# Kernel tuning notes

Measured on AMD Instinct MI355X. Metric: run time of the kernel, lower is better.

## Reference

```python
import jax, jax.numpy as jnp
import numpy as np

B, CIN, CINT, H, W = 2, 2048, 512, 96, 96
CQK = CINT // 8  # 64, mmcv CrissCrossAttention query/key channels
NG = 32          # GroupNorm groups
EPS = 1e-5


def conv1x1(x, w, b):
    # x: [B,C,H,W], w: [O,C,1,1], b: [O]
    y = jnp.einsum('bchw,oc->bohw', x, w[:, :, 0, 0])
    return y + b[None, :, None, None]


def conv3x3(x, w):
    return jax.lax.conv_general_dilated(
        x, w, window_strides=(1, 1), padding=((1, 1), (1, 1)),
        dimension_numbers=('NCHW', 'OIHW', 'NCHW'))


def group_norm(x, gamma, beta):
    b, c, h, w = x.shape
    xg = x.reshape(b, NG, c // NG, h, w)
    mu = xg.mean(axis=(2, 3, 4), keepdims=True)
    var = xg.var(axis=(2, 3, 4), keepdims=True)
    xg = (xg - mu) * jax.lax.rsqrt(var + EPS)
    return xg.reshape(b, c, h, w) * gamma[None, :, None, None] + beta[None, :, None, None]


def criss_cross_attention(x, qw, qb, kw, kb, vw, vb, gamma):
    # mmcv CrissCrossAttention: attention restricted to each pixel's row + column.
    b, c, h, w = x.shape
    q = conv1x1(x, qw, qb)  # [B,Cqk,H,W]
    k = conv1x1(x, kw, kb)  # [B,Cqk,H,W]
    v = conv1x1(x, vw, vb)  # [B,C,H,W]
    # column (H-direction) energy: e_H[b,h,w,i] = sum_c q[b,c,h,w] k[b,c,i,w]
    e_h = jnp.einsum('bchw,bciw->bhwi', q, k)
    diag = jnp.eye(h, dtype=bool)[:, None, :]  # mask i==h (self counted once, in W branch)
    e_h = jnp.where(diag, -jnp.inf, e_h)
    # row (W-direction) energy: e_W[b,h,w,j] = sum_c q[b,c,h,w] k[b,c,h,j]
    e_w = jnp.einsum('bchw,bchj->bhwj', q, k)
    attn = jax.nn.softmax(jnp.concatenate([e_h, e_w], axis=-1), axis=-1)  # [B,H,W,H+W]
    a_h, a_w = attn[..., :h], attn[..., h:]
    out = jnp.einsum('bciw,bhwi->bchw', v, a_h) + jnp.einsum('bchj,bhwj->bchw', v, a_w)
    return gamma * out + x


def setup_inputs() -> dict:
    key = jax.random.key(0)
    ks = jax.random.split(key, 12)
    s = 0.02
    return {
        'x': jax.random.normal(ks[0], (B, CIN, H, W), jnp.float32),
        'conv1_w': jax.random.normal(ks[1], (CINT, CIN, 1, 1), jnp.float32) * s,
        'conv1_b': jnp.zeros((CINT,), jnp.float32),
        'q_w': jax.random.normal(ks[2], (CQK, CINT, 1, 1), jnp.float32) * s,
        'q_b': jnp.zeros((CQK,), jnp.float32),
        'k_w': jax.random.normal(ks[3], (CQK, CINT, 1, 1), jnp.float32) * s,
        'k_b': jnp.zeros((CQK,), jnp.float32),
        'v_w': jax.random.normal(ks[4], (CINT, CINT, 1, 1), jnp.float32) * s,
        'v_b': jnp.zeros((CINT,), jnp.float32),
        'gamma': jnp.asarray(0.5, jnp.float32),
        'convout_w': jax.random.normal(ks[5], (CINT, CINT, 3, 3), jnp.float32) * s,
        'gn_gamma': jnp.ones((CINT,), jnp.float32),
        'gn_beta': jnp.zeros((CINT,), jnp.float32),
    }


def reference(x, conv1_w, conv1_b, q_w, q_b, k_w, k_b, v_w, v_b, gamma,
              convout_w, gn_gamma, gn_beta):
    out = conv1x1(x, conv1_w, conv1_b)
    for _ in range(2):  # recurrence = 2
        out = criss_cross_attention(out, q_w, q_b, k_w, k_b, v_w, v_b, gamma)
    out = conv3x3(out, convout_w)  # ConvModule with GN => conv has no bias
    out = group_norm(out, gn_gamma, gn_beta)
    return out
```

## Files before the change

kernel.cpp:

```cpp
#include <hip/hip_runtime.h>
#include <hip/hip_bf16.h>


typedef __bf16 bf8_t __attribute__((ext_vector_type(8)));
typedef float f32x4 __attribute__((ext_vector_type(4)));

union I4B8 { int4 i; bf8_t b; };

typedef const __attribute__((address_space(1))) void as1_cvoid;
typedef __attribute__((address_space(3))) void as3_void;
__device__ __forceinline__ void gload16(const void* g, void* l) {
  __builtin_amdgcn_global_load_lds((as1_cvoid*)g, (as3_void*)l, 16, 0, 0);
}
__device__ __forceinline__ int rot8(int c, int key) { return (c + key) & 7; }

__global__ __launch_bounds__(256) void cast_rot_k(const float* s, __bf16* d, int K8, int total8) {
  int idx = blockIdx.x * 256 + threadIdx.x;
  if (idx >= total8) return;
  int c8 = idx % K8, n = idx / K8;
  int pos = rot8(c8 & 7, n & 7);
  const float* sp = s + ((long long)n * K8 + c8) * 8;
  float4 a = *(const float4*)sp, b = *(const float4*)(sp + 4);
  I4B8 u;
  u.b[0] = (__bf16)a.x; u.b[1] = (__bf16)a.y; u.b[2] = (__bf16)a.z; u.b[3] = (__bf16)a.w;
  u.b[4] = (__bf16)b.x; u.b[5] = (__bf16)b.y; u.b[6] = (__bf16)b.z; u.b[7] = (__bf16)b.w;
  *(int4*)(d + ((long long)n * K8 + (c8 & ~7) + pos) * 8) = u.i;
}

__global__ __launch_bounds__(256) void wqkv_rot_k(const float* qw, const float* kw, const float* vw, __bf16* d) {
  int idx = blockIdx.x * 256 + threadIdx.x;
  if (idx >= 640 * 64) return;
  int c8 = idx & 63, n = idx >> 6;
  const float* src = (n < 64) ? qw + (long long)n * 512
                   : (n < 128) ? kw + (long long)(n - 64) * 512
                               : vw + (long long)(n - 128) * 512;
  int pos = rot8(c8 & 7, n & 7);
  const float* sp = src + c8 * 8;
  float4 a = *(const float4*)sp, b = *(const float4*)(sp + 4);
  I4B8 u;
  u.b[0] = (__bf16)a.x; u.b[1] = (__bf16)a.y; u.b[2] = (__bf16)a.z; u.b[3] = (__bf16)a.w;
  u.b[4] = (__bf16)b.x; u.b[5] = (__bf16)b.y; u.b[6] = (__bf16)b.z; u.b[7] = (__bf16)b.w;
  *(int4*)(d + ((long long)n * 64 + (c8 & ~7) + pos) * 8) = u.i;
}

__global__ __launch_bounds__(256) void fuse_bias_k(const float* qb, const float* kb, const float* vb,
                                                   float* d, float* stats) {
  int i = blockIdx.x * 256 + threadIdx.x;
  if (i < 128) stats[i] = 0.f;
  if (i >= 640) return;
  d[i] = (i < 64) ? qb[i] : (i < 128) ? kb[i - 64] : vb[i - 128];
}

__global__ __launch_bounds__(256) void reorder_w_k(const float* w, __bf16* wr) {
  __shared__ float ls[4608];
  int o = blockIdx.x;
  int t = threadIdx.x;
  const float* base = w + (long long)o * 4608;
#pragma unroll
  for (int i = 0; i < 18; i++) ls[t + i * 256] = base[t + i * 256];
  __syncthreads();
#pragma unroll
  for (int i = 0; i < 3; i++) {
    int q = t + i * 256;
    if (q >= 576) break;
    int k0 = q * 8;
    int dydx = k0 / 512, c0 = k0 & 511;
    I4B8 u;
#pragma unroll
    for (int j = 0; j < 8; j++) u.b[j] = (__bf16)ls[(c0 + j) * 9 + dydx];
    int pos = rot8((k0 >> 3) & 7, o & 7);
    *(int4*)(wr + (long long)o * 4608 + (k0 & ~63) + pos * 8) = u.i;
  }
}

__global__ __launch_bounds__(256) void transpose_x_k(const float* x, __bf16* xt) {
  __shared__ __bf16 l[64 * 66];
  int c0 = blockIdx.x * 64, s0 = blockIdx.y * 64, b = blockIdx.z;
  int t = threadIdx.x;
#pragma unroll
  for (int i = 0; i < 2; i++) {
    int slot = t + i * 256;
    int cl = slot >> 3, sch = slot & 7;
    const float* src = x + ((long long)(b * 2048 + c0 + cl)) * 9216 + s0 + sch * 8;
    float4 a = *(const float4*)src, bb = *(const float4*)(src + 4);
    __bf16* dst = &l[cl * 66 + sch * 8];
    dst[0] = (__bf16)a.x; dst[1] = (__bf16)a.y; dst[2] = (__bf16)a.z; dst[3] = (__bf16)a.w;
    dst[4] = (__bf16)bb.x; dst[5] = (__bf16)bb.y; dst[6] = (__bf16)bb.z; dst[7] = (__bf16)bb.w;
  }
  __syncthreads();
#pragma unroll
  for (int i = 0; i < 2; i++) {
    int slot = t + i * 256;
    int sl = slot >> 3, cch = slot & 7;
    I4B8 u;
#pragma unroll
    for (int j = 0; j < 8; j++) u.b[j] = l[(cch * 8 + j) * 66 + sl];
    *(int4*)(xt + ((long long)(b * 9216 + s0 + sl)) * 2048 + c0 + rot8(cch, sl & 7) * 8) = u.i;
  }
}

__global__ __launch_bounds__(256) void border0_k(__bf16* padb) {
  int idx = blockIdx.x * 256 + threadIdx.x;
  if (idx >= 776 * 64) return;
  int ch = idx & 63, bi = idx >> 6;
  int b = bi / 388, r = bi % 388;
  int hh, ww;
  if (r < 98) { hh = 0; ww = r; }
  else if (r < 196) { hh = 97; ww = r - 98; }
  else if (r < 292) { hh = r - 196 + 1; ww = 0; }
  else { hh = r - 292 + 1; ww = 97; }
  *(int4*)(padb + ((long long)(b * 9604 + hh * 98 + ww)) * 512 + ch * 8) = make_int4(0, 0, 0, 0);
}

struct GemmAP {
  const __bf16 *A, *B;
  __bf16* C;
  const float* bias;
  long long sAr, sBr, sCr;
  int K, ntn;
};

template <int CROT>
__global__ __launch_bounds__(256) void gemm_async_k(GemmAP p) {
  __shared__ __attribute__((aligned(16))) __bf16 lA[128 * 64];
  __shared__ __attribute__((aligned(16))) __bf16 lB[64 * 64];
  const int t = threadIdx.x;
  const int id = blockIdx.x;
  const int per8 = gridDim.x >> 3;
  const int lin = (id & 7) * per8 + (id >> 3);
  const int m0 = (lin / p.ntn) * 128, n0 = (lin % p.ntn) * 64;
  const int lane = t & 63, wave = t >> 6;
  const int wm = (wave >> 1) * 64, wn = (wave & 1) * 32;
  const int l15 = lane & 15, l4 = lane >> 4;
  const int srow = (lane >> 3), schunk = (lane & 7) * 8;
  f32x4 acc[4][2];
#pragma unroll
  for (int i = 0; i < 4; i++)
#pragma unroll
    for (int j = 0; j < 2; j++) acc[i][j] = f32x4{0.f, 0.f, 0.f, 0.f};

  for (int kb = 0; kb < p.K; kb += 64) {
    const int rbA = wave * 32, rbB = wave * 16;
#pragma unroll
    for (int i = 0; i < 4; i++) {
      int row = rbA + i * 8;
      gload16(p.A + (long long)(m0 + row + srow) * p.sAr + kb + schunk, &lA[row * 64]);
    }
#pragma unroll
    for (int i = 0; i < 2; i++) {
      int row = rbB + i * 8;
      gload16(p.B + (long long)(n0 + row + srow) * p.sBr + kb + schunk, &lB[row * 64]);
    }
    __syncthreads();
#pragma unroll
    for (int kk = 0; kk < 2; kk++) {
      bf8_t af[4], bfr[2];
      int cch = kk * 4 + l4;
#pragma unroll
      for (int mt = 0; mt < 4; mt++) {
        int r = wm + mt * 16 + l15;
        af[mt] = *(bf8_t*)&lA[r * 64 + (rot8(cch, r & 7) << 3)];
      }
#pragma unroll
      for (int nt = 0; nt < 2; nt++) {
        int r = wn + nt * 16 + l15;
        bfr[nt] = *(bf8_t*)&lB[r * 64 + (rot8(cch, r & 7) << 3)];
      }
#pragma unroll
      for (int mt = 0; mt < 4; mt++)
#pragma unroll
        for (int nt = 0; nt < 2; nt++)
          acc[mt][nt] = __builtin_amdgcn_mfma_f32_16x16x32_bf16(af[mt], bfr[nt], acc[mt][nt], 0, 0, 0);
    }
    __syncthreads();
  }
#pragma unroll
  for (int nt = 0; nt < 2; nt++) {
    int col = n0 + wn + nt * 16 + l15;
    float bv = p.bias[col];
#pragma unroll
    for (int mt = 0; mt < 4; mt++) {
      int row0 = m0 + wm + mt * 16 + (l4 << 2);
#pragma unroll
      for (int r = 0; r < 4; r++) {
        int row = row0 + r;
        int pc = CROT ? (col & ~63) + (rot8((col >> 3) & 7, row & 7) << 3) + (col & 7) : col;
        p.C[(long long)row * p.sCr + pc] = (__bf16)(acc[mt][nt][r] + bv);
      }
    }
  }
}

struct AggP {
  const __bf16 *A, *B;
  __bf16* C;
  const __bf16 *tmp, *res;
  const float* gma;
  long long bB1, bB2, sBr;
  long long cB1, cB2, sCr;
};

template <int MODE>
__global__ __launch_bounds__(256) void agg_k(AggP p) {
  __shared__ __attribute__((aligned(16))) __bf16 lA[128 * 64];
  __shared__ __attribute__((aligned(16))) __bf16 lB[128 * 64];
  const int t = threadIdx.x;
  const int z = blockIdx.z;
  const int z1 = z / 96, z2 = z % 96;
  const __bf16* A = p.A + (long long)z * (96 * 128);
  const __bf16* B = p.B + (long long)z1 * p.bB1 + (long long)z2 * p.bB2;
  const int n0 = blockIdx.x * 128;
  const int lane = t & 63, wave = t >> 6;
  const int wm = (wave >> 1) * 64, wn = (wave & 1) * 64;
  const int l15 = lane & 15, l4 = lane >> 4;
  const int srow = lane >> 3, schunk = (lane & 7) * 8;
  f32x4 acc[4][4];
#pragma unroll
  for (int i = 0; i < 4; i++)
#pragma unroll
    for (int j = 0; j < 4; j++) acc[i][j] = f32x4{0.f, 0.f, 0.f, 0.f};

#pragma unroll
  for (int kb = 0; kb < 128; kb += 64) {
    const int rb = wave * 32;
#pragma unroll
    for (int i = 0; i < 4; i++) {
      int row = rb + i * 8;
      gload16(A + (long long)(row + srow) * 128 + kb + schunk, &lA[row * 64]);
    }
#pragma unroll
    for (int i = 0; i < 4; i++) {
      int slot = t + i * 256;
      int kl = slot & 63, cch = slot >> 6;
      int gk = kb + kl;
      I4B8 u;
      u.i = make_int4(0, 0, 0, 0);
      if (gk < 96) u.i = *(const int4*)(B + (long long)gk * p.sBr + n0 + cch * 8);
#pragma unroll
      for (int j = 0; j < 8; j++) {
        int n = cch * 8 + j;
        lB[n * 64 + (rot8(kl >> 3, n & 7) << 3) + (kl & 7)] = u.b[j];
      }
    }
    __syncthreads();
#pragma unroll
    for (int kk = 0; kk < 2; kk++) {
      bf8_t af[4], bfr[4];
      int cch = kk * 4 + l4;
#pragma unroll
      for (int mt = 0; mt < 4; mt++) {
        int r = wm + mt * 16 + l15;
        af[mt] = *(bf8_t*)&lA[r * 64 + (rot8(cch, r & 7) << 3)];
      }
#pragma unroll
      for (int nt = 0; nt < 4; nt++) {
        int r = wn + nt * 16 + l15;
        bfr[nt] = *(bf8_t*)&lB[r * 64 + (rot8(cch, r & 7) << 3)];
      }
#pragma unroll
      for (int mt = 0; mt < 4; mt++)
#pragma unroll
        for (int nt = 0; nt < 4; nt++)
          acc[mt][nt] = __builtin_amdgcn_mfma_f32_16x16x32_bf16(af[mt], bfr[nt], acc[mt][nt], 0, 0, 0);
    }
    __syncthreads();
  }
  long long cbase = (long long)z1 * p.cB1 + (long long)z2 * p.cB2;
  float g = MODE ? *p.gma : 0.f;
#pragma unroll
  for (int nt = 0; nt < 4; nt++) {
    int col = n0 + wn + nt * 16 + l15;
#pragma unroll
    for (int mt = 0; mt < 4; mt++) {
      int row0 = wm + mt * 16 + (l4 << 2);
#pragma unroll
      for (int r = 0; r < 4; r++) {
        int row = row0 + r;
        if (row >= 96) continue;
        long long offL = cbase + (long long)row * p.sCr + col;
        float v = acc[mt][nt][r];
        if (MODE == 0) {
          p.C[offL] = (__bf16)v;
        } else {
          int rc = (col & ~63) + (rot8((col >> 3) & 7, row & 7) << 3) + (col & 7);
          long long offP = cbase + (long long)row * p.sCr + rc;
          v = g * ((float)p.tmp[offL] + v) + (float)p.res[offP];
          if (MODE == 1) {
            p.C[offP] = (__bf16)v;
          } else {
            int pc = (col & ~63) + (rot8((col >> 3) & 7, (row + 1) & 7) << 3) + (col & 7);
            long long pidx = (long long)z1 * 9604 + (long long)(z2 + 1) * 98 + (row + 1);
            p.C[pidx * 512 + pc] = (__bf16)v;
          }
        }
      }
    }
  }
}

__global__ __launch_bounds__(384) void cc_scores_k(const __bf16* qkv, float* attnfH, float* attnfW) {
  __shared__ __attribute__((aligned(16))) __bf16 Qs[96 * 64];
  __shared__ __attribute__((aligned(16))) __bf16 Ks[96 * 64];
  int bfi = blockIdx.x;
  int b = bfi / 96, f = bfi % 96;
  int mode = blockIdx.y;
  long long base = (mode == 0) ? ((long long)(b * 9216 + f)) * 640 : ((long long)(b * 9216 + f * 96)) * 640;
  long long rstr = (mode == 0) ? 96 * 640 : 640;
  int t = threadIdx.x;
#pragma unroll
  for (int i = 0; i < 2; i++) {
    int slot = t + i * 384;
    int r = slot >> 3, c = slot & 7;
    int sw = rot8(c, r & 7) << 3;
    *(int4*)&Qs[r * 64 + sw] = *(const int4*)(qkv + base + (long long)r * rstr + c * 8);
    *(int4*)&Ks[r * 64 + sw] = *(const int4*)(qkv + base + (long long)r * rstr + 64 + c * 8);
  }
  __syncthreads();
  int lane = t & 63, wave = t >> 6;
  int l15 = lane & 15, l4 = lane >> 4;
  f32x4 acc[6];
#pragma unroll
  for (int i = 0; i < 6; i++) acc[i] = f32x4{0.f, 0.f, 0.f, 0.f};
#pragma unroll
  for (int kk = 0; kk < 2; kk++) {
    int ar = wave * 16 + l15;
    int cch = kk * 4 + l4;
    bf8_t af = *(bf8_t*)&Qs[ar * 64 + (rot8(cch, ar & 7) << 3)];
#pragma unroll
    for (int nt = 0; nt < 6; nt++) {
      int br = nt * 16 + l15;
      bf8_t bfr = *(bf8_t*)&Ks[br * 64 + (rot8(cch, br & 7) << 3)];
      acc[nt] = __builtin_amdgcn_mfma_f32_16x16x32_bf16(af, bfr, acc[nt], 0, 0, 0);
    }
  }
  float* dst = (mode == 0 ? attnfH : attnfW) + (long long)bfi * 9216;
#pragma unroll
  for (int nt = 0; nt < 6; nt++) {
#pragma unroll
    for (int r = 0; r < 4; r++) {
      int m = wave * 16 + (l4 << 2) + r;
      int n = nt * 16 + l15;
      float v = acc[nt][r];
      if (mode == 0 && n == m) v = -__builtin_inff();
      dst[m * 96 + n] = v;
    }
  }
}

__global__ __launch_bounds__(256) void cc_softmax_k(const float* attnfH, const float* attnfW,
                                                    __bf16* a_h, __bf16* a_w) {
  int wave = threadIdx.x >> 6, lane = threadIdx.x & 63;
  int pix = blockIdx.x * 4 + wave;
  int b = pix / 9216, hw = pix % 9216;
  int h = hw / 96, w2 = hw % 96;
  const float* ehb = attnfH + ((long long)(b * 96 + w2)) * 9216 + h * 96;
  const float* ewb = attnfW + ((long long)(b * 96 + h)) * 9216 + w2 * 96;
  float x0 = ehb[lane];
  float x1 = lane < 32 ? ehb[64 + lane] : -__builtin_inff();
  float x2 = ewb[lane];
  float x3 = lane < 32 ? ewb[64 + lane] : -__builtin_inff();
  float m = fmaxf(fmaxf(x0, x1), fmaxf(x2, x3));
#pragma unroll
  for (int o = 32; o; o >>= 1) m = fmaxf(m, __shfl_xor(m, o));
  float e0 = __expf(x0 - m), e1 = __expf(x1 - m), e2 = __expf(x2 - m), e3 = __expf(x3 - m);
  float s = e0 + e1 + e2 + e3;
#pragma unroll
  for (int o = 32; o; o >>= 1) s += __shfl_xor(s, o);
  float inv = 1.f / s;
  __bf16* dh = a_h + ((long long)((b * 96 + w2) * 96 + h)) * 128;
  __bf16* dw = a_w + ((long long)((b * 96 + h) * 96 + w2)) * 128;
  int kh = h & 7, kw2 = w2 & 7;
  int k1 = lane, k2 = 64 + lane;
  int p1h = (k1 & ~63) + (rot8((k1 >> 3) & 7, kh) << 3) + (k1 & 7);
  int p2h = (k2 & ~63) + (rot8((k2 >> 3) & 7, kh) << 3) + (k2 & 7);
  int p1w = (k1 & ~63) + (rot8((k1 >> 3) & 7, kw2) << 3) + (k1 & 7);
  int p2w = (k2 & ~63) + (rot8((k2 >> 3) & 7, kw2) << 3) + (k2 & 7);
  dh[p1h] = (__bf16)(e0 * inv);
  dh[p2h] = (__bf16)(lane < 32 ? e1 * inv : 0.f);
  dw[p1w] = (__bf16)(e2 * inv);
  dw[p2w] = (__bf16)(lane < 32 ? e3 * inv : 0.f);
}

__global__ __launch_bounds__(256) void conv3_gemm_k(const __bf16* pin, const __bf16* wr, __bf16* C) {
  __shared__ __attribute__((aligned(16))) __bf16 lA[128 * 64];
  __shared__ __attribute__((aligned(16))) __bf16 lB[128 * 64];
  const int t = threadIdx.x;
  const int id = blockIdx.x;
  const int per8 = gridDim.x >> 3;
  const int lin = (id & 7) * per8 + (id >> 3);
  const int m0 = (lin >> 2) * 128, n0 = (lin & 3) * 128;
  const int lane = t & 63, wave = t >> 6;
  const int wm = (wave >> 1) * 64, wn = (wave & 1) * 64;
  const int l15 = lane & 15, l4 = lane >> 4;
  const int srow = lane >> 3, schunk = (lane & 7) * 8;
  const int rb = wave * 32;
  f32x4 acc[4][4];
#pragma unroll
  for (int i = 0; i < 4; i++)
#pragma unroll
    for (int j = 0; j < 4; j++) acc[i][j] = f32x4{0.f, 0.f, 0.f, 0.f};
  long long sbase[4], bbase[4];
#pragma unroll
  for (int i = 0; i < 4; i++) {
    int r = rb + i * 8 + srow;
    int m = m0 + r;
    int b = m / 9216, hw = m % 9216;
    int h = hw / 96, w2 = hw % 96;
    sbase[i] = ((long long)b * 9604 + h * 98 + w2) * 512 + schunk;
    bbase[i] = (long long)(n0 + r) * 4608 + schunk;
  }
  int w2f[4];
#pragma unroll
  for (int mt = 0; mt < 4; mt++) w2f[mt] = (m0 + wm + mt * 16 + l15) % 96;

  int kt = 0;
  for (int tap = 0; tap < 9; tap++) {
    const int dy = tap / 3, dx = tap - dy * 3;
    const long long aoff = (long long)(dy * 98 + dx) * 512;
    int keyA[4];
#pragma unroll
    for (int mt = 0; mt < 4; mt++) keyA[mt] = (w2f[mt] + dx) & 7;
    for (int sl = 0; sl < 8; sl++, kt++) {
      const int c0k = sl * 64;
#pragma unroll
      for (int i = 0; i < 4; i++) {
        gload16(pin + sbase[i] + aoff + c0k, &lA[(rb + i * 8) * 64]);
        gload16(wr + bbase[i] + kt * 64, &lB[(rb + i * 8) * 64]);
      }
      __syncthreads();
#pragma unroll
      for (int kk = 0; kk < 2; kk++) {
        bf8_t af[4], bfr[4];
        int cch = kk * 4 + l4;
#pragma unroll
        for (int mt = 0; mt < 4; mt++) {
          int r = wm + mt * 16 + l15;
          af[mt] = *(bf8_t*)&lA[r * 64 + (rot8(cch, keyA[mt]) << 3)];
        }
#pragma unroll
        for (int nt = 0; nt < 4; nt++) {
          int r = wn + nt * 16 + l15;
          bfr[nt] = *(bf8_t*)&lB[r * 64 + (rot8(cch, r & 7) << 3)];
        }
#pragma unroll
        for (int mt = 0; mt < 4; mt++)
#pragma unroll
          for (int nt = 0; nt < 4; nt++)
            acc[mt][nt] = __builtin_amdgcn_mfma_f32_16x16x32_bf16(af[mt], bfr[nt], acc[mt][nt], 0, 0, 0);
      }
      __syncthreads();
    }
  }
#pragma unroll
  for (int nt = 0; nt < 4; nt++) {
    int col = n0 + wn + nt * 16 + l15;
#pragma unroll
    for (int mt = 0; mt < 4; mt++) {
      int row0 = m0 + wm + mt * 16 + (l4 << 2);
#pragma unroll
      for (int r = 0; r < 4; r++) {
        int row = row0 + r;
        C[(long long)row * 512 + col] = (__bf16)acc[mt][nt][r];
      }
    }
  }
}

__global__ __launch_bounds__(256) void gn_stats_k(const __bf16* z, float* stats) {
  int bi = blockIdx.x, t = threadIdx.x;
  const __bf16* base = z + (long long)bi * (72 * 512);
  int g = (t & 63) >> 1;
  float s = 0.f, ss = 0.f;
#pragma unroll
  for (int i = 0; i < 18; i++) {
    I4B8 u;
    u.i = *(const int4*)(base + ((long long)(t + i * 256)) * 8);
#pragma unroll
    for (int j = 0; j < 8; j++) {
      float f = (float)u.b[j];
      s += f;
      ss += f * f;
    }
  }
  s += __shfl_xor(s, 1);
  ss += __shfl_xor(ss, 1);
  __shared__ float red[2][4][32];
  int wave = t >> 6, lane = t & 63;
  if (!(lane & 1)) {
    red[0][wave][g] = s;
    red[1][wave][g] = ss;
  }
  __syncthreads();
  if (t < 32) {
    float S = red[0][0][t] + red[0][1][t] + red[0][2][t] + red[0][3][t];
    float SS = red[1][0][t] + red[1][1][t] + red[1][2][t] + red[1][3][t];
    int b = bi >> 7;
    atomicAdd(&stats[2 * (b * 32 + t)], S);
    atomicAdd(&stats[2 * (b * 32 + t) + 1], SS);
  }
}

__global__ __launch_bounds__(256) void gn_write_k(const __bf16* z, const float* stats,
                                                 const float* gng, const float* gnb, float* out) {
  __shared__ __bf16 l[64 * 98];
  int c0 = blockIdx.x * 64, h = blockIdx.y, b = blockIdx.z;
  int t = threadIdx.x;
#pragma unroll
  for (int i = 0; i < 3; i++) {
    int slot = t + i * 256;
    int wl = slot >> 3, cch = slot & 7;
    I4B8 u;
    u.i = *(const int4*)(z + ((long long)(b * 9216 + h * 96 + wl)) * 512 + c0 + cch * 8);
#pragma unroll
    for (int j = 0; j < 8; j++) l[(cch * 8 + j) * 98 + wl] = u.b[j];
  }
  __syncthreads();
  const float inv = 1.f / 147456.f;
#pragma unroll
  for (int i = 0; i < 3; i++) {
    int slot = t + i * 256;
    int wch = slot % 12, cl = slot / 12;
    int c = c0 + cl;
    int g = c >> 4;
    float S = stats[2 * (b * 32 + g)], SS = stats[2 * (b * 32 + g) + 1];
    float mean = S * inv;
    float rstd = rsqrtf(SS * inv - mean * mean + 1e-5f);
    float sc = rstd * gng[c];
    float sh = gnb[c] - mean * sc;
    float4 o0, o1;
    const __bf16* src = &l[cl * 98 + wch * 8];
    o0.x = (float)src[0] * sc + sh; o0.y = (float)src[1] * sc + sh;
    o0.z = (float)src[2] * sc + sh; o0.w = (float)src[3] * sc + sh;
    o1.x = (float)src[4] * sc + sh; o1.y = (float)src[5] * sc + sh;
    o1.z = (float)src[6] * sc + sh; o1.w = (float)src[7] * sc + sh;
    float* dst = out + ((long long)((b * 512 + c) * 96 + h)) * 96 + wch * 8;
    *(float4*)dst = o0;
    *(float4*)(dst + 4) = o1;
  }
}

extern "C" void kernel_launch(void* const* d_in, const int* in_sizes, int n_in,
                              void* d_out, int out_size, void* d_ws, size_t ws_size,
                              hipStream_t stream) {
  (void)in_sizes; (void)n_in; (void)out_size;
  const float* x = (const float*)d_in[0];
  const float* conv1w = (const float*)d_in[1];
  const float* conv1b = (const float*)d_in[2];
  const float* qw = (const float*)d_in[3];
  const float* qbias = (const float*)d_in[4];
  const float* kw = (const float*)d_in[5];
  const float* kbias = (const float*)d_in[6];
  const float* vw = (const float*)d_in[7];
  const float* vbias = (const float*)d_in[8];
  const float* gma = (const float*)d_in[9];
  const float* cow = (const float*)d_in[10];
  const float* gng = (const float*)d_in[11];
  const float* gnb = (const float*)d_in[12];
  float* out = (float*)d_out;

  if (ws_size < 134876160ULL) return;

  char* w = (char*)d_ws;
  __bf16* xt     = (__bf16*)(w);
  __bf16* qkv    = (__bf16*)(w);
  float* attnfH  = (float*)(w + 23592960);
  float* attnfW  = (float*)(w + 30670848);
  __bf16* a_h    = (__bf16*)(w + 37748736);
  __bf16* a_w    = (__bf16*)(w + 42467328);
  __bf16* padb   = (__bf16*)(w + 47185920);
  __bf16* wrot   = (__bf16*)(w + 66854912);
  __bf16* ya     = (__bf16*)(w + 75497472);
  __bf16* yb     = (__bf16*)(w + 94371840);
  __bf16* tmp1   = (__bf16*)(w + 113246208);
  __bf16* zb     = (__bf16*)(w);
  __bf16* c1wb   = (__bf16*)(w + 132120576);
  __bf16* wqkvb  = (__bf16*)(w + 134217728);
  float* qkvbias = (float*)(w + 134873088);
  float* stats   = (float*)(w + 134875648);

  cast_rot_k<<<512, 256, 0, stream>>>(conv1w, c1wb, 256, 131072);
  wqkv_rot_k<<<160, 256, 0, stream>>>(qw, kw, vw, wqkvb);
  fuse_bias_k<<<3, 256, 0, stream>>>(qbias, kbias, vbias, qkvbias, stats);
  transpose_x_k<<<dim3(32, 144, 2), 256, 0, stream>>>(x, xt);

  {
    GemmAP p{};
    p.A = xt; p.B = c1wb; p.C = ya; p.bias = conv1b;
    p.sAr = 2048; p.sBr = 2048; p.sCr = 512;
    p.K = 2048; p.ntn = 8;
    gemm_async_k<1><<<1152, 256, 0, stream>>>(p);
  }

  for (int it = 0; it < 2; it++) {
    __bf16* tin = it ? yb : ya;
    {
      GemmAP p{};
      p.A = tin; p.B = wqkvb; p.C = qkv; p.bias = qkvbias;
      p.sAr = 512; p.sBr = 512; p.sCr = 640;
      p.K = 512; p.ntn = 10;
      gemm_async_k<0><<<1440, 256, 0, stream>>>(p);
    }
    cc_scores_k<<<dim3(192, 2), 384, 0, stream>>>(qkv, attnfH, attnfW);
    cc_softmax_k<<<4608, 256, 0, stream>>>(attnfH, attnfW, a_h, a_w);
    {
      AggP p{};
      p.A = a_h; p.B = qkv + 128; p.C = tmp1;
      p.bB1 = (long long)9216 * 640; p.bB2 = 640; p.sBr = (long long)96 * 640;
      p.cB1 = (long long)9216 * 512; p.cB2 = 512; p.sCr = (long long)96 * 512;
      agg_k<0><<<dim3(4, 1, 192), 256, 0, stream>>>(p);
    }
    {
      AggP p{};
      p.A = a_w; p.B = qkv + 128;
      p.bB1 = (long long)9216 * 640; p.bB2 = (long long)96 * 640; p.sBr = 640;
      p.cB1 = (long long)9216 * 512; p.cB2 = (long long)96 * 512; p.sCr = 512;
      p.tmp = tmp1; p.res = tin; p.gma = gma;
      if (it == 0) {
        p.C = yb;
        agg_k<1><<<dim3(4, 1, 192), 256, 0, stream>>>(p);
      } else {
        p.C = padb;
        agg_k<2><<<dim3(4, 1, 192), 256, 0, stream>>>(p);
      }
    }
  }

  reorder_w_k<<<512, 256, 0, stream>>>(cow, wrot);
  border0_k<<<194, 256, 0, stream>>>(padb);
  conv3_gemm_k<<<576, 256, 0, stream>>>(padb, wrot, zb);
  gn_stats_k<<<256, 256, 0, stream>>>(zb, stats);
  gn_write_k<<<dim3(8, 96, 2), 256, 0, stream>>>(zb, stats, gng, gnb, out);
}
```

Measured before the change: 619.1 us.

## Pre-transpose Q/K/V per column so column attention uses contiguous async loads

Adds a transpose kernel that writes per-column contiguous Q/K rows and a K-major, rotation-swizzled copy of V, padded to 128 along H. The column-direction score kernel now reads Q/K contiguously instead of with a 96×640-element stride. The column aggregation GEMM loads its B tile with async global-to-LDS copies instead of per-element scattered LDS writes. The cost is an extra kernel and extra memory traffic. The new buffers alias workspace regions (a_h, padb), and the V copy's size may extend past padb into the next region.

Result: slower. 633.2 us (+2.3%).

```diff
diff --git a/kernel.cpp b/kernel.cpp
--- a/kernel.cpp
+++ b/kernel.cpp
@@ -110,6 +110,49 @@
   else if (r < 292) { hh = r - 196 + 1; ww = 0; }
   else { hh = r - 292 + 1; ww = 97; }
   *(int4*)(padb + ((long long)(b * 9604 + hh * 98 + ww)) * 512 + ch * 8) = make_int4(0, 0, 0, 0);
+}
+
+__global__ __launch_bounds__(256) void vtrans_k(const __bf16* qkv, __bf16* qkvT, __bf16* vt1) {
+  int bw = blockIdx.x;
+  int b = bw / 96, w2 = bw % 96;
+  int t = threadIdx.x;
+  const __bf16* src = qkv + ((long long)(b * 9216) + w2) * 640;
+  int mode = blockIdx.y;
+  if (mode == 0) {
+#pragma unroll
+    for (int i = 0; i < 6; i++) {
+      int slot = t + i * 256;
+      int h = slot >> 4, c8 = slot & 15;
+      int4 u = *(const int4*)(src + (long long)h * (96 * 640) + c8 * 8);
+      *(int4*)(qkvT + ((long long)bw * 96 + h) * 128 + c8 * 8) = u;
+    }
+    return;
+  }
+  int half = mode - 1;
+  __shared__ __bf16 l[96 * 256];
+#pragma unroll
+  for (int i = 0; i < 12; i++) {
+    int slot = t + i * 256;
+    int h = slot >> 5, c8 = slot & 31;
+    int4 u = *(const int4*)(src + (long long)h * (96 * 640) + 128 + half * 256 + c8 * 8);
+    *(int4*)&l[h * 256 + ((c8 ^ ((h >> 3) & 7)) << 3)] = u;
+  }
+  __syncthreads();
+  __bf16* dst = vt1 + (long long)bw * (512 * 128) + (long long)half * (256 * 128);
+#pragma unroll
+  for (int i = 0; i < 16; i++) {
+    int slot = t + i * 256;
+    int cl = slot >> 4, kc = slot & 15;
+    int c = half * 256 + cl;
+    I4B8 u;
+#pragma unroll
+    for (int j = 0; j < 8; j++) {
+      int h = kc * 8 + j;
+      u.b[j] = (h < 96) ? l[h * 256 + ((((cl >> 3) ^ (kc & 7)) << 3) | (cl & 7))] : (__bf16)0.f;
+    }
+    int pos = (kc & ~7) + rot8(kc & 7, c & 7);
+    *(int4*)(dst + (long long)cl * 128 + pos * 8) = u.i;
+  }
 }
 
 struct GemmAP {
@@ -228,18 +271,27 @@
       int row = rb + i * 8;
       gload16(A + (long long)(row + srow) * 128 + kb + schunk, &lA[row * 64]);
     }
-#pragma unroll
-    for (int i = 0; i < 4; i++) {
-      int slot = t + i * 256;
-      int kl = slot & 63, cch = slot >> 6;
-      int gk = kb + kl;
-      I4B8 u;
-      u.i = make_int4(0, 0, 0, 0);
-      if (gk < 96) u.i = *(const int4*)(B + (long long)gk * p.sBr + n0 + cch * 8);
-#pragma unroll
-      for (int j = 0; j < 8; j++) {
-        int n = cch * 8 + j;
-        lB[n * 64 + (rot8(kl >> 3, n & 7) << 3) + (kl & 7)] = u.b[j];
+    if (MODE == 0) {
+      const __bf16* Bn = B + (long long)n0 * 128;
+#pragma unroll
+      for (int i = 0; i < 4; i++) {
+        int row = rb + i * 8;
+        gload16(Bn + (long long)(row + srow) * 128 + kb + schunk, &lB[row * 64]);
+      }
+    } else {
+#pragma unroll
+      for (int i = 0; i < 4; i++) {
+        int slot = t + i * 256;
+        int kl = slot & 63, cch = slot >> 6;
+        int gk = kb + kl;
+        I4B8 u;
+        u.i = make_int4(0, 0, 0, 0);
+        if (gk < 96) u.i = *(const int4*)(B + (long long)gk * p.sBr + n0 + cch * 8);
+#pragma unroll
+        for (int j = 0; j < 8; j++) {
+          int n = cch * 8 + j;
+          lB[n * 64 + (rot8(kl >> 3, n & 7) << 3) + (kl & 7)] = u.b[j];
+        }
       }
     }
     __syncthreads();
@@ -298,22 +350,25 @@
   }
 }
 
-__global__ __launch_bounds__(384) void cc_scores_k(const __bf16* qkv, float* attnfH, float* attnfW) {
+__global__ __launch_bounds__(384) void cc_scores_k(const __bf16* qkv, const __bf16* qkvT,
+                                                   float* attnfH, float* attnfW) {
   __shared__ __attribute__((aligned(16))) __bf16 Qs[96 * 64];
   __shared__ __attribute__((aligned(16))) __bf16 Ks[96 * 64];
   int bfi = blockIdx.x;
   int b = bfi / 96, f = bfi % 96;
   int mode = blockIdx.y;
-  long long base = (mode == 0) ? ((long long)(b * 9216 + f)) * 640 : ((long long)(b * 9216 + f * 96)) * 640;
-  long long rstr = (mode == 0) ? 96 * 640 : 640;
+  const __bf16* srcb;
+  long long rstr;
+  if (mode == 0) { srcb = qkvT + (long long)bfi * (96 * 128); rstr = 128; }
+  else { srcb = qkv + ((long long)(b * 9216 + f * 96)) * 640; rstr = 640; }
   int t = threadIdx.x;
 #pragma unroll
   for (int i = 0; i < 2; i++) {
     int slot = t + i * 384;
     int r = slot >> 3, c = slot & 7;
     int sw = rot8(c, r & 7) << 3;
-    *(int4*)&Qs[r * 64 + sw] = *(const int4*)(qkv + base + (long long)r * rstr + c * 8);
-    *(int4*)&Ks[r * 64 + sw] = *(const int4*)(qkv + base + (long long)r * rstr + 64 + c * 8);
+    *(int4*)&Qs[r * 64 + sw] = *(const int4*)(srcb + (long long)r * rstr + c * 8);
+    *(int4*)&Ks[r * 64 + sw] = *(const int4*)(srcb + (long long)r * rstr + 64 + c * 8);
   }
   __syncthreads();
   int lane = t & 63, wave = t >> 6;
@@ -566,8 +621,10 @@
   float* attnfH  = (float*)(w + 23592960);
   float* attnfW  = (float*)(w + 30670848);
   __bf16* a_h    = (__bf16*)(w + 37748736);
+  __bf16* qkvT   = (__bf16*)(w + 37748736);
   __bf16* a_w    = (__bf16*)(w + 42467328);
   __bf16* padb   = (__bf16*)(w + 47185920);
+  __bf16* vt1    = (__bf16*)(w + 47185920);
   __bf16* wrot   = (__bf16*)(w + 66854912);
   __bf16* ya     = (__bf16*)(w + 75497472);
   __bf16* yb     = (__bf16*)(w + 94371840);
@@ -600,12 +657,13 @@
       p.K = 512; p.ntn = 10;
       gemm_async_k<0><<<1440, 256, 0, stream>>>(p);
     }
-    cc_scores_k<<<dim3(192, 2), 384, 0, stream>>>(qkv, attnfH, attnfW);
+    vtrans_k<<<dim3(192, 3), 256, 0, stream>>>(qkv, qkvT, vt1);
+    cc_scores_k<<<dim3(192, 2), 384, 0, stream>>>(qkv, qkvT, attnfH, attnfW);
     cc_softmax_k<<<4608, 256, 0, stream>>>(attnfH, attnfW, a_h, a_w);
     {
       AggP p{};
-      p.A = a_h; p.B = qkv + 128; p.C = tmp1;
-      p.bB1 = (long long)9216 * 640; p.bB2 = 640; p.sBr = (long long)96 * 640;
+      p.A = a_h; p.B = vt1; p.C = tmp1;
+      p.bB1 = (long long)96 * 512 * 128; p.bB2 = (long long)512 * 128; p.sBr = 128;
       p.cB1 = (long long)9216 * 512; p.cB2 = 512; p.sCr = (long long)96 * 512;
       agg_k<0><<<dim3(4, 1, 192), 256, 0, stream>>>(p);
     }
```

## Double-buffer LDS tiles in GEMM and conv3x3 kernels with async prefetch

Applied to the files above, without the earlier changes.

Both the generic 1x1 GEMM kernel and the implicit-GEMM 3x3 conv kernel now keep two LDS buffers. Each iteration issues the global-to-LDS loads for the next K slice, then waits only for the current slice with a partial vmcnt. This lets memory latency overlap with MFMA work and drops one full barrier per step. The cost is doubled LDS use (up to 64KB for conv3), which may lower occupancy. Correctness also depends on the hand-written vmcnt counts matching the number of loads issued per stage.

Measured after the change: 693.2 us. +12.0%, slower.

```diff
diff --git a/kernel.cpp b/kernel.cpp
--- a/kernel.cpp
+++ b/kernel.cpp
@@ -122,8 +122,8 @@
 
 template <int CROT>
 __global__ __launch_bounds__(256) void gemm_async_k(GemmAP p) {
-  __shared__ __attribute__((aligned(16))) __bf16 lA[128 * 64];
-  __shared__ __attribute__((aligned(16))) __bf16 lB[64 * 64];
+  __shared__ __attribute__((aligned(16))) __bf16 lA[2][128 * 64];
+  __shared__ __attribute__((aligned(16))) __bf16 lB[2][64 * 64];
   const int t = threadIdx.x;
   const int id = blockIdx.x;
   const int per8 = gridDim.x >> 3;
@@ -133,25 +133,36 @@
   const int wm = (wave >> 1) * 64, wn = (wave & 1) * 32;
   const int l15 = lane & 15, l4 = lane >> 4;
   const int srow = (lane >> 3), schunk = (lane & 7) * 8;
+  const int rbA = wave * 32, rbB = wave * 16;
   f32x4 acc[4][2];
 #pragma unroll
   for (int i = 0; i < 4; i++)
 #pragma unroll
     for (int j = 0; j < 2; j++) acc[i][j] = f32x4{0.f, 0.f, 0.f, 0.f};
 
-  for (int kb = 0; kb < p.K; kb += 64) {
-    const int rbA = wave * 32, rbB = wave * 16;
+  auto stage = [&](int bu, int kb) {
 #pragma unroll
     for (int i = 0; i < 4; i++) {
       int row = rbA + i * 8;
-      gload16(p.A + (long long)(m0 + row + srow) * p.sAr + kb + schunk, &lA[row * 64]);
+      gload16(p.A + (long long)(m0 + row + srow) * p.sAr + kb + schunk, &lA[bu][row * 64]);
     }
 #pragma unroll
     for (int i = 0; i < 2; i++) {
       int row = rbB + i * 8;
-      gload16(p.B + (long long)(n0 + row + srow) * p.sBr + kb + schunk, &lB[row * 64]);
-    }
-    __syncthreads();
+      gload16(p.B + (long long)(n0 + row + srow) * p.sBr + kb + schunk, &lB[bu][row * 64]);
+    }
+  };
+
+  stage(0, 0);
+  int bu = 0;
+  for (int kb = 0; kb < p.K; kb += 64) {
+    if (kb + 64 < p.K) {
+      stage(bu ^ 1, kb + 64);
+      asm volatile("s_waitcnt vmcnt(6)" ::: "memory");
+    } else {
+      asm volatile("s_waitcnt vmcnt(0)" ::: "memory");
+    }
+    __builtin_amdgcn_s_barrier();
 #pragma unroll
     for (int kk = 0; kk < 2; kk++) {
       bf8_t af[4], bfr[2];
@@ -159,12 +170,12 @@
 #pragma unroll
       for (int mt = 0; mt < 4; mt++) {
         int r = wm + mt * 16 + l15;
-        af[mt] = *(bf8_t*)&lA[r * 64 + (rot8(cch, r & 7) << 3)];
+        af[mt] = *(bf8_t*)&lA[bu][r * 64 + (rot8(cch, r & 7) << 3)];
       }
 #pragma unroll
       for (int nt = 0; nt < 2; nt++) {
         int r = wn + nt * 16 + l15;
-        bfr[nt] = *(bf8_t*)&lB[r * 64 + (rot8(cch, r & 7) << 3)];
+        bfr[nt] = *(bf8_t*)&lB[bu][r * 64 + (rot8(cch, r & 7) << 3)];
       }
 #pragma unroll
       for (int mt = 0; mt < 4; mt++)
@@ -172,7 +183,8 @@
         for (int nt = 0; nt < 2; nt++)
           acc[mt][nt] = __builtin_amdgcn_mfma_f32_16x16x32_bf16(af[mt], bfr[nt], acc[mt][nt], 0, 0, 0);
     }
-    __syncthreads();
+    if (kb + 64 < p.K) __builtin_amdgcn_s_barrier();
+    bu ^= 1;
   }
 #pragma unroll
   for (int nt = 0; nt < 2; nt++) {
@@ -382,8 +394,8 @@
 }
 
 __global__ __launch_bounds__(256) void conv3_gemm_k(const __bf16* pin, const __bf16* wr, __bf16* C) {
-  __shared__ __attribute__((aligned(16))) __bf16 lA[128 * 64];
-  __shared__ __attribute__((aligned(16))) __bf16 lB[128 * 64];
+  __shared__ __attribute__((aligned(16))) __bf16 lA[2][128 * 64];
+  __shared__ __attribute__((aligned(16))) __bf16 lB[2][128 * 64];
   const int t = threadIdx.x;
   const int id = blockIdx.x;
   const int per8 = gridDim.x >> 3;
@@ -413,43 +425,55 @@
 #pragma unroll
   for (int mt = 0; mt < 4; mt++) w2f[mt] = (m0 + wm + mt * 16 + l15) % 96;
 
-  int kt = 0;
-  for (int tap = 0; tap < 9; tap++) {
-    const int dy = tap / 3, dx = tap - dy * 3;
-    const long long aoff = (long long)(dy * 98 + dx) * 512;
+  auto stage = [&](int bu, int kt2) {
+    int tap = kt2 >> 3, sl = kt2 & 7;
+    int dyq = tap / 3;
+    long long aoff = (long long)(dyq * 98 + (tap - dyq * 3)) * 512;
+    int c0k = sl * 64;
+#pragma unroll
+    for (int i = 0; i < 4; i++) {
+      gload16(pin + sbase[i] + aoff + c0k, &lA[bu][(rb + i * 8) * 64]);
+      gload16(wr + bbase[i] + kt2 * 64, &lB[bu][(rb + i * 8) * 64]);
+    }
+  };
+
+  stage(0, 0);
+  int bu = 0;
+  for (int kt = 0; kt < 72; kt++) {
+    if (kt < 71) {
+      stage(bu ^ 1, kt + 1);
+      asm volatile("s_waitcnt vmcnt(8)" ::: "memory");
+    } else {
+      asm volatile("s_waitcnt vmcnt(0)" ::: "memory");
+    }
+    __builtin_amdgcn_s_barrier();
+    int tap = kt >> 3;
+    int dx = tap - (tap / 3) * 3;
     int keyA[4];
 #pragma unroll
     for (int mt = 0; mt < 4; mt++) keyA[mt] = (w2f[mt] + dx) & 7;
-    for (int sl = 0; sl < 8; sl++, kt++) {
-      const int c0k = sl * 64;
-#pragma unroll
-      for (int i = 0; i < 4; i++) {
-        gload16(pin + sbase[i] + aoff + c0k, &lA[(rb + i * 8) * 64]);
-        gload16(wr + bbase[i] + kt * 64, &lB[(rb + i * 8) * 64]);
-      }
-      __syncthreads();
-#pragma unroll
-      for (int kk = 0; kk < 2; kk++) {
-        bf8_t af[4], bfr[4];
-        int cch = kk * 4 + l4;
-#pragma unroll
-        for (int mt = 0; mt < 4; mt++) {
-          int r = wm + mt * 16 + l15;
-          af[mt] = *(bf8_t*)&lA[r * 64 + (rot8(cch, keyA[mt]) << 3)];
-        }
-#pragma unroll
-        for (int nt = 0; nt < 4; nt++) {
-          int r = wn + nt * 16 + l15;
-          bfr[nt] = *(bf8_t*)&lB[r * 64 + (rot8(cch, r & 7) << 3)];
-        }
-#pragma unroll
-        for (int mt = 0; mt < 4; mt++)
-#pragma unroll
-          for (int nt = 0; nt < 4; nt++)
-            acc[mt][nt] = __builtin_amdgcn_mfma_f32_16x16x32_bf16(af[mt], bfr[nt], acc[mt][nt], 0, 0, 0);
-      }
-      __syncthreads();
-    }
+#pragma unroll
+    for (int kk = 0; kk < 2; kk++) {
+      bf8_t af[4], bfr[4];
+      int cch = kk * 4 + l4;
+#pragma unroll
+      for (int mt = 0; mt < 4; mt++) {
+        int r = wm + mt * 16 + l15;
+        af[mt] = *(bf8_t*)&lA[bu][r * 64 + (rot8(cch, keyA[mt]) << 3)];
+      }
+#pragma unroll
+      for (int nt = 0; nt < 4; nt++) {
+        int r = wn + nt * 16 + l15;
+        bfr[nt] = *(bf8_t*)&lB[bu][r * 64 + (rot8(cch, r & 7) << 3)];
+      }
+#pragma unroll
+      for (int mt = 0; mt < 4; mt++)
+#pragma unroll
+        for (int nt = 0; nt < 4; nt++)
+          acc[mt][nt] = __builtin_amdgcn_mfma_f32_16x16x32_bf16(af[mt], bfr[nt], acc[mt][nt], 0, 0, 0);
+    }
+    if (kt < 71) __builtin_amdgcn_s_barrier();
+    bu ^= 1;
   }
 #pragma unroll
   for (int nt = 0; nt < 4; nt++) {
```
